# Performance work log

Measured on AMD Instinct MI355X. Metric: run time of the kernel, lower is better.

The kernel has to match this reference:

```python
import jax, jax.numpy as jnp
import numpy as np

N_NODES = 131072
N_EDGES = 2097152
IN_DIM = 768
HID = 64
NODES_PER_GRAPH = 32
OUT_DIM = 2


def setup_inputs() -> dict:
    key = jax.random.key(0)
    k1, k2, k3, k4 = jax.random.split(key, 4)
    x = jax.random.normal(k1, (N_NODES, IN_DIM), dtype=jnp.float32)
    edge_index = jax.random.randint(k2, (2, N_EDGES), 0, N_NODES, dtype=jnp.int64)
    W_conv = jax.random.normal(k3, (IN_DIM, HID), dtype=jnp.float32) * 0.02
    b_conv = jnp.zeros((HID,), dtype=jnp.float32)
    W_lin = jax.random.normal(k4, (OUT_DIM, HID * NODES_PER_GRAPH), dtype=jnp.float32) * 0.02
    b_lin = jnp.zeros((OUT_DIM,), dtype=jnp.float32)
    return {"x": x, "edge_index": edge_index, "W_conv": W_conv,
            "b_conv": b_conv, "W_lin": W_lin, "b_lin": b_lin}


def reference(x, edge_index, W_conv, b_conv, W_lin, b_lin):
    N = x.shape[0]
    # GCNConv: add self-loops, symmetric normalization D^-1/2 (A+I) D^-1/2
    loops = jnp.arange(N, dtype=edge_index.dtype)
    src = jnp.concatenate([edge_index[0], loops])  # [E+N]
    dst = jnp.concatenate([edge_index[1], loops])
    deg = jax.ops.segment_sum(jnp.ones_like(dst, dtype=x.dtype), dst, num_segments=N)
    dinv = jax.lax.rsqrt(deg)  # deg >= 1 due to self-loops
    norm = dinv[src] * dinv[dst]  # [E+N]
    h = x @ W_conv  # [N, HID]
    msg = h[src] * norm[:, None]  # gather + scale
    out = jax.ops.segment_sum(msg, dst, num_segments=N) + b_conv  # scatter-add
    out = jax.nn.relu(out)
    out = out.reshape(-1, HID * NODES_PER_GRAPH)  # [B, 2048]
    logits = out @ W_lin.T + b_lin  # [B, OUT_DIM]
    return jax.nn.log_softmax(logits, axis=1)
```

## Files before the change

### kernel.cpp

```cpp
#include <hip/hip_runtime.h>
#include <hip/hip_bf16.h>

#define N_NODES 131072
#define N_EDGES 2097152
#define IN_DIM 768
#define HID 64
#define NPG 32
#define NGRAPH (N_NODES / NPG)

#define BM 128
#define KC 32
#define NT (IN_DIM / KC)
#define GEMM_BLOCKS (N_NODES / BM)

#define RNG 128
#define NB (N_NODES / RNG)
#define EPB 4096
#define NCB (N_EDGES / EPB)
#define PBLK 8
#define RPB (NCB / PBLK)
#define PREP_BLK 192

typedef __attribute__((ext_vector_type(8))) short bf16x8;
typedef __attribute__((ext_vector_type(4))) float f32x4;

static __device__ __forceinline__ unsigned short f2bf(float f) {
    __hip_bfloat16 h = __float2bfloat16(f);
    return *reinterpret_cast<unsigned short*>(&h);
}
static __device__ __forceinline__ float bf2f(unsigned short s) {
    return __uint_as_float(((unsigned int)s) << 16);
}

static __device__ __forceinline__ void gload_lds16(const float* g, float* l) {
    __builtin_amdgcn_global_load_lds(
        (const __attribute__((address_space(1))) void*)g,
        (__attribute__((address_space(3))) void*)l, 16, 0, 0);
}

__global__ __launch_bounds__(256) void gcn_prep_count(const float* __restrict__ W,
                                                      unsigned short* __restrict__ Wt,
                                                      const int* __restrict__ dst,
                                                      unsigned int* __restrict__ C) {
    __shared__ unsigned int hist[NB];
    int tid = threadIdx.x;
    if (blockIdx.x < PREP_BLK) {
        int i = blockIdx.x * 256 + tid;
        if (i < IN_DIM * HID) {
            int k = i >> 6, n = i & 63;
            Wt[n * IN_DIM + k] = f2bf(W[i]);
        }
        return;
    }
    int cb = blockIdx.x - PREP_BLK;
    for (int t = tid; t < NB; t += 256) hist[t] = 0u;
    __syncthreads();
    int base = cb * EPB;
    #pragma unroll
    for (int u = 0; u < EPB / 256; ++u) {
        int d = dst[base + u * 256 + tid];
        atomicAdd(&hist[d >> 7], 1u);
    }
    __syncthreads();
    for (int t = tid; t < NB; t += 256) C[(size_t)cb * NB + t] = hist[t];
}

__global__ __launch_bounds__(256) void gcn_prefA(unsigned int* __restrict__ C,
                                                 unsigned int* __restrict__ S) {
    int tid = threadIdx.x;
    int p = blockIdx.x;
    #pragma unroll
    for (int c = 0; c < 4; ++c) {
        int t = tid + c * 256;
        unsigned int run = 0;
        for (int r = 0; r < RPB; r += 8) {
            unsigned int v[8];
            size_t base = ((size_t)(p * RPB + r)) * NB + t;
            #pragma unroll
            for (int j = 0; j < 8; ++j) v[j] = C[base + (size_t)j * NB];
            #pragma unroll
            for (int j = 0; j < 8; ++j) { C[base + (size_t)j * NB] = run; run += v[j]; }
        }
        S[p * NB + t] = run;
    }
}

__global__ __launch_bounds__(256) void gcn_prefB(unsigned int* __restrict__ S,
                                                 unsigned int* __restrict__ bstart) {
    __shared__ unsigned int sm[256];
    int tid = threadIdx.x;
    unsigned int lexcl[4];
    unsigned int lrun = 0;
    #pragma unroll
    for (int j = 0; j < 4; ++j) {
        unsigned int t = tid * 4 + j;
        unsigned int r = 0;
        #pragma unroll
        for (int p = 0; p < PBLK; ++p) {
            unsigned int v = S[p * NB + t];
            S[p * NB + t] = r;
            r += v;
        }
        lexcl[j] = lrun;
        lrun += r;
    }
    sm[tid] = lrun;
    __syncthreads();
    for (int off = 1; off < 256; off <<= 1) {
        unsigned int u = (tid >= off) ? sm[tid - off] : 0u;
        __syncthreads();
        sm[tid] += u;
        __syncthreads();
    }
    unsigned int texcl = sm[tid] - lrun;
    #pragma unroll
    for (int j = 0; j < 4; ++j) bstart[tid * 4 + j] = texcl + lexcl[j];
    if (tid == 255) bstart[NB] = N_EDGES;
}

__global__ __launch_bounds__(256) void gcn_scatter(const int* __restrict__ src,
                                                   const int* __restrict__ dst,
                                                   const unsigned int* __restrict__ C,
                                                   const unsigned int* __restrict__ S,
                                                   const unsigned int* __restrict__ bstart,
                                                   unsigned int* __restrict__ part) {
    __shared__ unsigned int off[NB];
    int tid = threadIdx.x, cb = blockIdx.x;
    int p = cb >> 6;
    for (int t = tid; t < NB; t += 256)
        off[t] = bstart[t] + S[p * NB + t] + C[(size_t)cb * NB + t];
    __syncthreads();
    int base = cb * EPB;
    #pragma unroll
    for (int u = 0; u < EPB / 256; ++u) {
        int i = base + u * 256 + tid;
        int d = dst[i];
        unsigned int pos = atomicAdd(&off[d >> 7], 1u);
        part[pos] = (unsigned int)src[i] | ((unsigned int)(d & (RNG - 1)) << 17);
    }
}

__global__ __launch_bounds__(256) void gcn_sort2(const unsigned int* __restrict__ part,
                                                 const unsigned int* __restrict__ bstart,
                                                 unsigned int* __restrict__ part2,
                                                 unsigned int* __restrict__ nstart,
                                                 float* __restrict__ dinv) {
    __shared__ unsigned int hist[RNG];
    __shared__ unsigned int sc[RNG];
    __shared__ unsigned int off[RNG];
    int tid = threadIdx.x, b = blockIdx.x;
    if (tid < RNG) hist[tid] = 0u;
    __syncthreads();
    unsigned int s0 = bstart[b], s1 = bstart[b + 1];
    for (unsigned int j = s0 + tid; j < s1; j += 256)
        atomicAdd(&hist[part[j] >> 17], 1u);
    __syncthreads();
    if (tid < RNG) sc[tid] = hist[tid];
    __syncthreads();
    #pragma unroll
    for (int o = 1; o < RNG; o <<= 1) {
        unsigned int u = (tid < RNG && tid >= o) ? sc[tid - o] : 0u;
        __syncthreads();
        if (tid < RNG) sc[tid] += u;
        __syncthreads();
    }
    if (tid < RNG) {
        unsigned int excl = sc[tid] - hist[tid];
        nstart[b * RNG + tid] = s0 + excl;
        off[tid] = s0 + excl;
        dinv[b * RNG + tid] = rsqrtf((float)(hist[tid] + 1));
    }
    if (b == NB - 1 && tid == 0) nstart[N_NODES] = N_EDGES;
    __syncthreads();
    for (unsigned int j = s0 + tid; j < s1; j += 256) {
        unsigned int pr = part[j];
        unsigned int pos = atomicAdd(&off[pr >> 17], 1u);
        part2[pos] = pr & 0x1FFFF;
    }
}

__global__ __launch_bounds__(256) void gcn_gemm(const float* __restrict__ x,
                                                const unsigned short* __restrict__ Wt,
                                                const float* __restrict__ dinv,
                                                unsigned short* __restrict__ hsb) {
    __shared__ __align__(16) float xs[2][BM][KC];
    int tid = threadIdx.x;
    int lane = tid & 63;
    int w = tid >> 6;
    int rowbase = blockIdx.x * BM;
    int rl = lane & 15;
    int kq = (lane >> 4) * 8;

    int jhi = lane >> 3, jlo = lane & 7;
    int cg = jlo ^ jhi;
    const float* gbase = x + (size_t)rowbase * IN_DIM + cg * 4;
    const unsigned short* wp = Wt + (size_t)rl * IN_DIM + kq;

    int r0 = w * 32 + rl, r1 = r0 + 16;
    int swz = rl & 7;
    int G0 = (lane >> 4) * 2;

    f32x4 acc[2][4] = {};

    #pragma unroll
    for (int q = 0; q < 4; ++q) {
        int segq = w * 4 + q;
        gload_lds16(gbase + (size_t)(segq * 8 + jhi) * IN_DIM, &xs[0][segq * 8][0]);
    }
    __syncthreads();

    for (int t = 0; t < NT; ++t) {
        int cur = t & 1;
        if (t + 1 < NT) {
            #pragma unroll
            for (int q = 0; q < 4; ++q) {
                int segq = w * 4 + q;
                gload_lds16(gbase + (size_t)(segq * 8 + jhi) * IN_DIM + (t + 1) * KC,
                            &xs[cur ^ 1][segq * 8][0]);
            }
        }
        const float4* xsf = (const float4*)xs[cur];
        float4 p0 = xsf[r0 * 8 + (G0 ^ swz)];
        float4 p1 = xsf[r0 * 8 + ((G0 + 1) ^ swz)];
        float4 p2 = xsf[r1 * 8 + (G0 ^ swz)];
        float4 p3 = xsf[r1 * 8 + ((G0 + 1) ^ swz)];
        int kb = t * KC;
        bf16x8 b0 = *(const bf16x8*)(wp + kb);
        bf16x8 b1 = *(const bf16x8*)(wp + (size_t)16 * IN_DIM + kb);
        bf16x8 b2 = *(const bf16x8*)(wp + (size_t)32 * IN_DIM + kb);
        bf16x8 b3 = *(const bf16x8*)(wp + (size_t)48 * IN_DIM + kb);
        bf16x8 a0, a1;
        a0[0] = (short)f2bf(p0.x); a0[1] = (short)f2bf(p0.y);
        a0[2] = (short)f2bf(p0.z); a0[3] = (short)f2bf(p0.w);
        a0[4] = (short)f2bf(p1.x); a0[5] = (short)f2bf(p1.y);
        a0[6] = (short)f2bf(p1.z); a0[7] = (short)f2bf(p1.w);
        a1[0] = (short)f2bf(p2.x); a1[1] = (short)f2bf(p2.y);
        a1[2] = (short)f2bf(p2.z); a1[3] = (short)f2bf(p2.w);
        a1[4] = (short)f2bf(p3.x); a1[5] = (short)f2bf(p3.y);
        a1[6] = (short)f2bf(p3.z); a1[7] = (short)f2bf(p3.w);
        acc[0][0] = __builtin_amdgcn_mfma_f32_16x16x32_bf16(a0, b0, acc[0][0], 0, 0, 0);
        acc[1][0] = __builtin_amdgcn_mfma_f32_16x16x32_bf16(a1, b0, acc[1][0], 0, 0, 0);
        acc[0][1] = __builtin_amdgcn_mfma_f32_16x16x32_bf16(a0, b1, acc[0][1], 0, 0, 0);
        acc[1][1] = __builtin_amdgcn_mfma_f32_16x16x32_bf16(a1, b1, acc[1][1], 0, 0, 0);
        acc[0][2] = __builtin_amdgcn_mfma_f32_16x16x32_bf16(a0, b2, acc[0][2], 0, 0, 0);
        acc[1][2] = __builtin_amdgcn_mfma_f32_16x16x32_bf16(a1, b2, acc[1][2], 0, 0, 0);
        acc[0][3] = __builtin_amdgcn_mfma_f32_16x16x32_bf16(a0, b3, acc[0][3], 0, 0, 0);
        acc[1][3] = __builtin_amdgcn_mfma_f32_16x16x32_bf16(a1, b3, acc[1][3], 0, 0, 0);
        __syncthreads();
    }
    #pragma unroll
    for (int rt = 0; rt < 2; ++rt) {
        int row0 = rowbase + w * 32 + rt * 16 + (lane >> 4) * 4;
        #pragma unroll
        for (int rr = 0; rr < 4; ++rr) {
            float dv = dinv[row0 + rr];
            #pragma unroll
            for (int ct = 0; ct < 4; ++ct) {
                int col = ct * 16 + rl;
                hsb[(size_t)(row0 + rr) * HID + col] = f2bf(acc[rt][ct][rr] * dv);
            }
        }
    }
}

__global__ __launch_bounds__(512) void gcn_agg(const unsigned short* __restrict__ hsb,
                                               const unsigned int* __restrict__ part2,
                                               const unsigned int* __restrict__ nstart,
                                               const float* __restrict__ dinv,
                                               const float* __restrict__ b_conv,
                                               const float* __restrict__ W_lin,
                                               const float* __restrict__ b_lin,
                                               float* __restrict__ out) {
    __shared__ float p0s[8], p1s[8];
    int tid = threadIdx.x, lane = tid & 63, w = tid >> 6;
    int g = blockIdx.x;
    float bc = b_conv[lane];
    float l0 = 0.f, l1 = 0.f;

    int i0 = g * NPG + w * 4;
    int cc[4];
    unsigned int stt[4];
    float dii[4];
    int sidx[4];
    float av[4];
    #pragma unroll
    for (int k = 0; k < 4; ++k) {
        int i = i0 + k;
        unsigned int st = nstart[i], en = nstart[i + 1];
        stt[k] = st;
        cc[k] = (int)(en - st);
        dii[k] = dinv[i];
    }
    #pragma unroll
    for (int k = 0; k < 4; ++k)
        sidx[k] = (lane < cc[k]) ? (int)part2[stt[k] + lane] : (i0 + k);
    #pragma unroll
    for (int k = 0; k < 4; ++k)
        av[k] = bf2f(hsb[(size_t)(i0 + k) * HID + lane]);

    int cmax = max(max(cc[0], cc[1]), max(cc[2], cc[3]));
    int clim = min(cmax, 64);
    for (int e = 0; e < clim; e += 4) {
        float v[4][4];
        #pragma unroll
        for (int k = 0; k < 4; ++k) {
            #pragma unroll
            for (int j = 0; j < 4; ++j) {
                int idx = e + j;
                int cl = idx < cc[k] ? idx : 0;
                int s = __shfl(sidx[k], cl);
                v[k][j] = bf2f(hsb[(size_t)s * HID + lane]);
            }
        }
        #pragma unroll
        for (int k = 0; k < 4; ++k) {
            #pragma unroll
            for (int j = 0; j < 4; ++j)
                if (e + j < cc[k]) av[k] += v[k][j];
        }
    }
    #pragma unroll
    for (int k = 0; k < 4; ++k)
        for (int e2 = 64; e2 < cc[k]; ++e2)
            av[k] += bf2f(hsb[(size_t)part2[stt[k] + e2] * HID + lane]);

    #pragma unroll
    for (int k = 0; k < 4; ++k) {
        int node = w * 4 + k;
        float v = fmaxf(fmaf(av[k], dii[k], bc), 0.f);
        l0 = fmaf(v, W_lin[node * HID + lane], l0);
        l1 = fmaf(v, W_lin[HID * NPG + node * HID + lane], l1);
    }
    #pragma unroll
    for (int d = 32; d > 0; d >>= 1) {
        l0 += __shfl_down(l0, d);
        l1 += __shfl_down(l1, d);
    }
    if (lane == 0) { p0s[w] = l0; p1s[w] = l1; }
    __syncthreads();
    if (tid == 0) {
        float A = b_lin[0], B = b_lin[1];
        #pragma unroll
        for (int j = 0; j < 8; ++j) { A += p0s[j]; B += p1s[j]; }
        float m = fmaxf(A, B);
        float lse = m + logf(expf(A - m) + expf(B - m));
        out[g * 2 + 0] = A - lse;
        out[g * 2 + 1] = B - lse;
    }
}

extern "C" void kernel_launch(void* const* d_in, const int* in_sizes, int n_in,
                              void* d_out, int out_size, void* d_ws, size_t ws_size,
                              hipStream_t stream) {
    const float* x  = (const float*)d_in[0];
    const int* ei   = (const int*)d_in[1];
    const float* Wc = (const float*)d_in[2];
    const float* bc = (const float*)d_in[3];
    const float* Wl = (const float*)d_in[4];
    const float* bl = (const float*)d_in[5];
    float* out = (float*)d_out;

    char* ws = (char*)d_ws;
    unsigned short* Wt   = (unsigned short*)(ws);
    float*          dinv = (float*)(ws + (128 << 10));
    unsigned int*  bstart= (unsigned int*)(ws + (640 << 10));
    unsigned int*  S     = (unsigned int*)(ws + (656 << 10));
    unsigned int*  part2 = (unsigned int*)(ws + (1u << 20));
    unsigned int*  nstart= (unsigned int*)(ws + (9u << 20));
    unsigned int*  C     = (unsigned int*)(ws + (10u << 20));
    unsigned int*  part  = (unsigned int*)(ws + (12u << 20));
    unsigned short* hsb  = (unsigned short*)(ws + (10u << 20));

    const int* srcIdx = ei;
    const int* dstIdx = ei + N_EDGES;

    gcn_prep_count<<<PREP_BLK + NCB, 256, 0, stream>>>(Wc, Wt, dstIdx, C);
    gcn_prefA<<<PBLK, 256, 0, stream>>>(C, S);
    gcn_prefB<<<1, 256, 0, stream>>>(S, bstart);
    gcn_scatter<<<NCB, 256, 0, stream>>>(srcIdx, dstIdx, C, S, bstart, part);
    gcn_sort2<<<NB, 256, 0, stream>>>(part, bstart, part2, nstart, dinv);
    gcn_gemm<<<GEMM_BLOCKS, 256, 0, stream>>>(x, Wt, dinv, hsb);
    gcn_agg<<<NGRAPH, 512, 0, stream>>>(hsb, part2, nstart, dinv, bc, Wl, bl, out);
}
```

Baseline: 227.4 us.

## Overlap GEMM halves with scatter and sort kernels via block-split fusion

The GEMM no longer scales its output rows by dinv, so it no longer depends on the sort pass. Its 1024 blocks are split into two halves, and each half is co-launched in one kernel with the scatter and sort2 work respectively, so the edge bucketing overlaps with the x@W compute. The source-side dinv scaling moves into the aggregation kernel: each lane fetches dinv for its neighbor and shuffles it alongside the index, which adds a gather per edge. hsb is relocated in the workspace so it no longer aliases C and part, which are live during the fused kernels.

```diff
diff --git a/kernel.cpp b/kernel.cpp
--- a/kernel.cpp
+++ b/kernel.cpp
@@ -12,6 +12,7 @@
 #define KC 32
 #define NT (IN_DIM / KC)
 #define GEMM_BLOCKS (N_NODES / BM)
+#define GSPLIT 512
 
 #define RNG 128
 #define NB (N_NODES / RNG)
@@ -38,156 +39,14 @@
         (__attribute__((address_space(3))) void*)l, 16, 0, 0);
 }
 
-__global__ __launch_bounds__(256) void gcn_prep_count(const float* __restrict__ W,
-                                                      unsigned short* __restrict__ Wt,
-                                                      const int* __restrict__ dst,
-                                                      unsigned int* __restrict__ C) {
-    __shared__ unsigned int hist[NB];
-    int tid = threadIdx.x;
-    if (blockIdx.x < PREP_BLK) {
-        int i = blockIdx.x * 256 + tid;
-        if (i < IN_DIM * HID) {
-            int k = i >> 6, n = i & 63;
-            Wt[n * IN_DIM + k] = f2bf(W[i]);
-        }
-        return;
-    }
-    int cb = blockIdx.x - PREP_BLK;
-    for (int t = tid; t < NB; t += 256) hist[t] = 0u;
-    __syncthreads();
-    int base = cb * EPB;
-    #pragma unroll
-    for (int u = 0; u < EPB / 256; ++u) {
-        int d = dst[base + u * 256 + tid];
-        atomicAdd(&hist[d >> 7], 1u);
-    }
-    __syncthreads();
-    for (int t = tid; t < NB; t += 256) C[(size_t)cb * NB + t] = hist[t];
-}
-
-__global__ __launch_bounds__(256) void gcn_prefA(unsigned int* __restrict__ C,
-                                                 unsigned int* __restrict__ S) {
-    int tid = threadIdx.x;
-    int p = blockIdx.x;
-    #pragma unroll
-    for (int c = 0; c < 4; ++c) {
-        int t = tid + c * 256;
-        unsigned int run = 0;
-        for (int r = 0; r < RPB; r += 8) {
-            unsigned int v[8];
-            size_t base = ((size_t)(p * RPB + r)) * NB + t;
-            #pragma unroll
-            for (int j = 0; j < 8; ++j) v[j] = C[base + (size_t)j * NB];
-            #pragma unroll
-            for (int j = 0; j < 8; ++j) { C[base + (size_t)j * NB] = run; run += v[j]; }
-        }
-        S[p * NB + t] = run;
-    }
-}
-
-__global__ __launch_bounds__(256) void gcn_prefB(unsigned int* __restrict__ S,
-                                                 unsigned int* __restrict__ bstart) {
-    __shared__ unsigned int sm[256];
-    int tid = threadIdx.x;
-    unsigned int lexcl[4];
-    unsigned int lrun = 0;
-    #pragma unroll
-    for (int j = 0; j < 4; ++j) {
-        unsigned int t = tid * 4 + j;
-        unsigned int r = 0;
-        #pragma unroll
-        for (int p = 0; p < PBLK; ++p) {
-            unsigned int v = S[p * NB + t];
-            S[p * NB + t] = r;
-            r += v;
-        }
-        lexcl[j] = lrun;
-        lrun += r;
-    }
-    sm[tid] = lrun;
-    __syncthreads();
-    for (int off = 1; off < 256; off <<= 1) {
-        unsigned int u = (tid >= off) ? sm[tid - off] : 0u;
-        __syncthreads();
-        sm[tid] += u;
-        __syncthreads();
-    }
-    unsigned int texcl = sm[tid] - lrun;
-    #pragma unroll
-    for (int j = 0; j < 4; ++j) bstart[tid * 4 + j] = texcl + lexcl[j];
-    if (tid == 255) bstart[NB] = N_EDGES;
-}
-
-__global__ __launch_bounds__(256) void gcn_scatter(const int* __restrict__ src,
-                                                   const int* __restrict__ dst,
-                                                   const unsigned int* __restrict__ C,
-                                                   const unsigned int* __restrict__ S,
-                                                   const unsigned int* __restrict__ bstart,
-                                                   unsigned int* __restrict__ part) {
-    __shared__ unsigned int off[NB];
-    int tid = threadIdx.x, cb = blockIdx.x;
-    int p = cb >> 6;
-    for (int t = tid; t < NB; t += 256)
-        off[t] = bstart[t] + S[p * NB + t] + C[(size_t)cb * NB + t];
-    __syncthreads();
-    int base = cb * EPB;
-    #pragma unroll
-    for (int u = 0; u < EPB / 256; ++u) {
-        int i = base + u * 256 + tid;
-        int d = dst[i];
-        unsigned int pos = atomicAdd(&off[d >> 7], 1u);
-        part[pos] = (unsigned int)src[i] | ((unsigned int)(d & (RNG - 1)) << 17);
-    }
-}
-
-__global__ __launch_bounds__(256) void gcn_sort2(const unsigned int* __restrict__ part,
-                                                 const unsigned int* __restrict__ bstart,
-                                                 unsigned int* __restrict__ part2,
-                                                 unsigned int* __restrict__ nstart,
-                                                 float* __restrict__ dinv) {
-    __shared__ unsigned int hist[RNG];
-    __shared__ unsigned int sc[RNG];
-    __shared__ unsigned int off[RNG];
-    int tid = threadIdx.x, b = blockIdx.x;
-    if (tid < RNG) hist[tid] = 0u;
-    __syncthreads();
-    unsigned int s0 = bstart[b], s1 = bstart[b + 1];
-    for (unsigned int j = s0 + tid; j < s1; j += 256)
-        atomicAdd(&hist[part[j] >> 17], 1u);
-    __syncthreads();
-    if (tid < RNG) sc[tid] = hist[tid];
-    __syncthreads();
-    #pragma unroll
-    for (int o = 1; o < RNG; o <<= 1) {
-        unsigned int u = (tid < RNG && tid >= o) ? sc[tid - o] : 0u;
-        __syncthreads();
-        if (tid < RNG) sc[tid] += u;
-        __syncthreads();
-    }
-    if (tid < RNG) {
-        unsigned int excl = sc[tid] - hist[tid];
-        nstart[b * RNG + tid] = s0 + excl;
-        off[tid] = s0 + excl;
-        dinv[b * RNG + tid] = rsqrtf((float)(hist[tid] + 1));
-    }
-    if (b == NB - 1 && tid == 0) nstart[N_NODES] = N_EDGES;
-    __syncthreads();
-    for (unsigned int j = s0 + tid; j < s1; j += 256) {
-        unsigned int pr = part[j];
-        unsigned int pos = atomicAdd(&off[pr >> 17], 1u);
-        part2[pos] = pr & 0x1FFFF;
-    }
-}
-
-__global__ __launch_bounds__(256) void gcn_gemm(const float* __restrict__ x,
-                                                const unsigned short* __restrict__ Wt,
-                                                const float* __restrict__ dinv,
-                                                unsigned short* __restrict__ hsb) {
-    __shared__ __align__(16) float xs[2][BM][KC];
+static __device__ __forceinline__ void dev_gemm_dbuf(int gb, const float* x,
+                                                     const unsigned short* Wt,
+                                                     unsigned short* hsb,
+                                                     float* xs) {
     int tid = threadIdx.x;
     int lane = tid & 63;
     int w = tid >> 6;
-    int rowbase = blockIdx.x * BM;
+    int rowbase = gb * BM;
     int rl = lane & 15;
     int kq = (lane >> 4) * 8;
 
@@ -205,21 +64,22 @@
     #pragma unroll
     for (int q = 0; q < 4; ++q) {
         int segq = w * 4 + q;
-        gload_lds16(gbase + (size_t)(segq * 8 + jhi) * IN_DIM, &xs[0][segq * 8][0]);
+        gload_lds16(gbase + (size_t)(segq * 8 + jhi) * IN_DIM, xs + segq * 8 * KC);
     }
     __syncthreads();
 
     for (int t = 0; t < NT; ++t) {
         int cur = t & 1;
         if (t + 1 < NT) {
+            float* bufn = xs + (cur ^ 1) * (BM * KC);
             #pragma unroll
             for (int q = 0; q < 4; ++q) {
                 int segq = w * 4 + q;
                 gload_lds16(gbase + (size_t)(segq * 8 + jhi) * IN_DIM + (t + 1) * KC,
-                            &xs[cur ^ 1][segq * 8][0]);
+                            bufn + segq * 8 * KC);
             }
         }
-        const float4* xsf = (const float4*)xs[cur];
+        const float4* xsf = (const float4*)(xs + cur * (BM * KC));
         float4 p0 = xsf[r0 * 8 + (G0 ^ swz)];
         float4 p1 = xsf[r0 * 8 + ((G0 + 1) ^ swz)];
         float4 p2 = xsf[r1 * 8 + (G0 ^ swz)];
@@ -252,14 +112,184 @@
     for (int rt = 0; rt < 2; ++rt) {
         int row0 = rowbase + w * 32 + rt * 16 + (lane >> 4) * 4;
         #pragma unroll
-        for (int rr = 0; rr < 4; ++rr) {
-            float dv = dinv[row0 + rr];
-            #pragma unroll
-            for (int ct = 0; ct < 4; ++ct) {
+        for (int ct = 0; ct < 4; ++ct)
+            #pragma unroll
+            for (int rr = 0; rr < 4; ++rr) {
                 int col = ct * 16 + rl;
-                hsb[(size_t)(row0 + rr) * HID + col] = f2bf(acc[rt][ct][rr] * dv);
+                hsb[(size_t)(row0 + rr) * HID + col] = f2bf(acc[rt][ct][rr]);
             }
-        }
+    }
+}
+
+static __device__ __forceinline__ void dev_scatter(int cb, const int* src, const int* dst,
+                                                   const unsigned int* C, const unsigned int* S,
+                                                   const unsigned int* bstart,
+                                                   unsigned int* part, unsigned int* off) {
+    int tid = threadIdx.x;
+    int p = cb >> 6;
+    for (int t = tid; t < NB; t += 256)
+        off[t] = bstart[t] + S[p * NB + t] + C[(size_t)cb * NB + t];
+    __syncthreads();
+    int base = cb * EPB;
+    #pragma unroll
+    for (int u = 0; u < EPB / 256; ++u) {
+        int i = base + u * 256 + tid;
+        int d = dst[i];
+        unsigned int pos = atomicAdd(&off[d >> 7], 1u);
+        part[pos] = (unsigned int)src[i] | ((unsigned int)(d & (RNG - 1)) << 17);
+    }
+}
+
+static __device__ __forceinline__ void dev_sort2(int b, const unsigned int* part,
+                                                 const unsigned int* bstart,
+                                                 unsigned int* part2, unsigned int* nstart,
+                                                 float* dinv, unsigned int* sm) {
+    unsigned int* hist = sm;
+    unsigned int* sc   = sm + RNG;
+    unsigned int* off  = sm + 2 * RNG;
+    int tid = threadIdx.x;
+    if (tid < RNG) hist[tid] = 0u;
+    __syncthreads();
+    unsigned int s0 = bstart[b], s1 = bstart[b + 1];
+    for (unsigned int j = s0 + tid; j < s1; j += 256)
+        atomicAdd(&hist[part[j] >> 17], 1u);
+    __syncthreads();
+    if (tid < RNG) sc[tid] = hist[tid];
+    __syncthreads();
+    #pragma unroll
+    for (int o = 1; o < RNG; o <<= 1) {
+        unsigned int u = (tid < RNG && tid >= o) ? sc[tid - o] : 0u;
+        __syncthreads();
+        if (tid < RNG) sc[tid] += u;
+        __syncthreads();
+    }
+    if (tid < RNG) {
+        unsigned int excl = sc[tid] - hist[tid];
+        nstart[b * RNG + tid] = s0 + excl;
+        off[tid] = s0 + excl;
+        dinv[b * RNG + tid] = rsqrtf((float)(hist[tid] + 1));
+    }
+    if (b == NB - 1 && tid == 0) nstart[N_NODES] = N_EDGES;
+    __syncthreads();
+    for (unsigned int j = s0 + tid; j < s1; j += 256) {
+        unsigned int pr = part[j];
+        unsigned int pos = atomicAdd(&off[pr >> 17], 1u);
+        part2[pos] = pr & 0x1FFFF;
+    }
+}
+
+__global__ __launch_bounds__(256) void gcn_prep_count(const float* __restrict__ W,
+                                                      unsigned short* __restrict__ Wt,
+                                                      const int* __restrict__ dst,
+                                                      unsigned int* __restrict__ C) {
+    __shared__ unsigned int hist[NB];
+    int tid = threadIdx.x;
+    if (blockIdx.x < PREP_BLK) {
+        int i = blockIdx.x * 256 + tid;
+        if (i < IN_DIM * HID) {
+            int k = i >> 6, n = i & 63;
+            Wt[n * IN_DIM + k] = f2bf(W[i]);
+        }
+        return;
+    }
+    int cb = blockIdx.x - PREP_BLK;
+    for (int t = tid; t < NB; t += 256) hist[t] = 0u;
+    __syncthreads();
+    int base = cb * EPB;
+    #pragma unroll
+    for (int u = 0; u < EPB / 256; ++u) {
+        int d = dst[base + u * 256 + tid];
+        atomicAdd(&hist[d >> 7], 1u);
+    }
+    __syncthreads();
+    for (int t = tid; t < NB; t += 256) C[(size_t)cb * NB + t] = hist[t];
+}
+
+__global__ __launch_bounds__(256) void gcn_prefA(unsigned int* __restrict__ C,
+                                                 unsigned int* __restrict__ S) {
+    int tid = threadIdx.x;
+    int p = blockIdx.x;
+    #pragma unroll
+    for (int c = 0; c < 4; ++c) {
+        int t = tid + c * 256;
+        unsigned int run = 0;
+        for (int r = 0; r < RPB; r += 8) {
+            unsigned int v[8];
+            size_t base = ((size_t)(p * RPB + r)) * NB + t;
+            #pragma unroll
+            for (int j = 0; j < 8; ++j) v[j] = C[base + (size_t)j * NB];
+            #pragma unroll
+            for (int j = 0; j < 8; ++j) { C[base + (size_t)j * NB] = run; run += v[j]; }
+        }
+        S[p * NB + t] = run;
+    }
+}
+
+__global__ __launch_bounds__(256) void gcn_prefB(unsigned int* __restrict__ S,
+                                                 unsigned int* __restrict__ bstart) {
+    __shared__ unsigned int sm[256];
+    int tid = threadIdx.x;
+    unsigned int lexcl[4];
+    unsigned int lrun = 0;
+    #pragma unroll
+    for (int j = 0; j < 4; ++j) {
+        unsigned int t = tid * 4 + j;
+        unsigned int r = 0;
+        #pragma unroll
+        for (int p = 0; p < PBLK; ++p) {
+            unsigned int v = S[p * NB + t];
+            S[p * NB + t] = r;
+            r += v;
+        }
+        lexcl[j] = lrun;
+        lrun += r;
+    }
+    sm[tid] = lrun;
+    __syncthreads();
+    for (int off = 1; off < 256; off <<= 1) {
+        unsigned int u = (tid >= off) ? sm[tid - off] : 0u;
+        __syncthreads();
+        sm[tid] += u;
+        __syncthreads();
+    }
+    unsigned int texcl = sm[tid] - lrun;
+    #pragma unroll
+    for (int j = 0; j < 4; ++j) bstart[tid * 4 + j] = texcl + lexcl[j];
+    if (tid == 255) bstart[NB] = N_EDGES;
+}
+
+__global__ __launch_bounds__(256) void gcn_fusedA(const float* __restrict__ x,
+                                                  const unsigned short* __restrict__ Wt,
+                                                  unsigned short* __restrict__ hsb,
+                                                  const int* __restrict__ src,
+                                                  const int* __restrict__ dst,
+                                                  const unsigned int* __restrict__ C,
+                                                  const unsigned int* __restrict__ S,
+                                                  const unsigned int* __restrict__ bstart,
+                                                  unsigned int* __restrict__ part) {
+    __shared__ __align__(16) float smem[2 * BM * KC];
+    if ((int)blockIdx.x < GSPLIT) {
+        dev_gemm_dbuf(blockIdx.x, x, Wt, hsb, smem);
+    } else {
+        dev_scatter(blockIdx.x - GSPLIT, src, dst, C, S, bstart, part,
+                    (unsigned int*)smem);
+    }
+}
+
+__global__ __launch_bounds__(256) void gcn_fusedB(const float* __restrict__ x,
+                                                  const unsigned short* __restrict__ Wt,
+                                                  unsigned short* __restrict__ hsb,
+                                                  const unsigned int* __restrict__ part,
+                                                  const unsigned int* __restrict__ bstart,
+                                                  unsigned int* __restrict__ part2,
+                                                  unsigned int* __restrict__ nstart,
+                                                  float* __restrict__ dinv) {
+    __shared__ __align__(16) float smem[2 * BM * KC];
+    if ((int)blockIdx.x < GSPLIT) {
+        dev_gemm_dbuf(GSPLIT + blockIdx.x, x, Wt, hsb, smem);
+    } else {
+        dev_sort2(blockIdx.x - GSPLIT, part, bstart, part2, nstart, dinv,
+                  (unsigned int*)smem);
     }
 }
 
@@ -282,6 +312,7 @@
     unsigned int stt[4];
     float dii[4];
     int sidx[4];
+    float dsv[4];
     float av[4];
     #pragma unroll
     for (int k = 0; k < 4; ++k) {
@@ -292,11 +323,13 @@
         dii[k] = dinv[i];
     }
     #pragma unroll
+    for (int k = 0; k < 4; ++k) {
+        sidx[k] = (lane < cc[k]) ? (int)part2[stt[k] + lane] : (i0 + k);
+        dsv[k] = (lane < cc[k]) ? dinv[sidx[k]] : 0.f;
+    }
+    #pragma unroll
     for (int k = 0; k < 4; ++k)
-        sidx[k] = (lane < cc[k]) ? (int)part2[stt[k] + lane] : (i0 + k);
-    #pragma unroll
-    for (int k = 0; k < 4; ++k)
-        av[k] = bf2f(hsb[(size_t)(i0 + k) * HID + lane]);
+        av[k] = dii[k] * bf2f(hsb[(size_t)(i0 + k) * HID + lane]);
 
     int cmax = max(max(cc[0], cc[1]), max(cc[2], cc[3]));
     int clim = min(cmax, 64);
@@ -309,7 +342,8 @@
                 int idx = e + j;
                 int cl = idx < cc[k] ? idx : 0;
                 int s = __shfl(sidx[k], cl);
-                v[k][j] = bf2f(hsb[(size_t)s * HID + lane]);
+                float ds = __shfl(dsv[k], cl);
+                v[k][j] = ds * bf2f(hsb[(size_t)s * HID + lane]);
             }
         }
         #pragma unroll
@@ -321,8 +355,10 @@
     }
     #pragma unroll
     for (int k = 0; k < 4; ++k)
-        for (int e2 = 64; e2 < cc[k]; ++e2)
-            av[k] += bf2f(hsb[(size_t)part2[stt[k] + e2] * HID + lane]);
+        for (int e2 = 64; e2 < cc[k]; ++e2) {
+            int s = (int)part2[stt[k] + e2];
+            av[k] += dinv[s] * bf2f(hsb[(size_t)s * HID + lane]);
+        }
 
     #pragma unroll
     for (int k = 0; k < 4; ++k) {
@@ -361,15 +397,15 @@
     float* out = (float*)d_out;
 
     char* ws = (char*)d_ws;
-    unsigned short* Wt   = (unsigned short*)(ws);
-    float*          dinv = (float*)(ws + (128 << 10));
-    unsigned int*  bstart= (unsigned int*)(ws + (640 << 10));
-    unsigned int*  S     = (unsigned int*)(ws + (656 << 10));
-    unsigned int*  part2 = (unsigned int*)(ws + (1u << 20));
-    unsigned int*  nstart= (unsigned int*)(ws + (9u << 20));
-    unsigned int*  C     = (unsigned int*)(ws + (10u << 20));
-    unsigned int*  part  = (unsigned int*)(ws + (12u << 20));
-    unsigned short* hsb  = (unsigned short*)(ws + (10u << 20));
+    unsigned short* Wt    = (unsigned short*)(ws);
+    float*          dinv  = (float*)(ws + (128 << 10));
+    unsigned int*  bstart = (unsigned int*)(ws + (640 << 10));
+    unsigned int*  S      = (unsigned int*)(ws + (656 << 10));
+    unsigned int*  part2  = (unsigned int*)(ws + (1u << 20));
+    unsigned int*  nstart = (unsigned int*)(ws + (9u << 20));
+    unsigned int*  C      = (unsigned int*)(ws + (10u << 20));
+    unsigned int*  part   = (unsigned int*)(ws + (12u << 20));
+    unsigned short* hsb   = (unsigned short*)(ws + (20u << 20));
 
     const int* srcIdx = ei;
     const int* dstIdx = ei + N_EDGES;
@@ -377,8 +413,9 @@
     gcn_prep_count<<<PREP_BLK + NCB, 256, 0, stream>>>(Wc, Wt, dstIdx, C);
     gcn_prefA<<<PBLK, 256, 0, stream>>>(C, S);
     gcn_prefB<<<1, 256, 0, stream>>>(S, bstart);
-    gcn_scatter<<<NCB, 256, 0, stream>>>(srcIdx, dstIdx, C, S, bstart, part);
-    gcn_sort2<<<NB, 256, 0, stream>>>(part, bstart, part2, nstart, dinv);
-    gcn_gemm<<<GEMM_BLOCKS, 256, 0, stream>>>(x, Wt, dinv, hsb);
+    gcn_fusedA<<<GSPLIT + NCB, 256, 0, stream>>>(x, Wt, hsb, srcIdx, dstIdx,
+                                                 C, S, bstart, part);
+    gcn_fusedB<<<GSPLIT + NB, 256, 0, stream>>>(x, Wt, hsb, part, bstart,
+                                                part2, nstart, dinv);
     gcn_agg<<<NGRAPH, 512, 0, stream>>>(hsb, part2, nstart, dinv, bc, Wl, bl, out);
 }
```

New measurement: 251.2 us. 10.4% more time.
